# Kernel optimization log

Hardware: AMD Instinct MI355X
Metric: run time of the kernel (lower is better)

## Reference

```python
import jax, jax.numpy as jnp
import numpy as np


def setup_inputs() -> dict:
    key = jax.random.key(0)
    kq, kk, kv = jax.random.split(key, 3)
    B, L, H, E = 4, 2048, 16, 64
    return {
        "queries": jax.random.normal(kq, (B, L, H, E), dtype=jnp.float32),
        "keys": jax.random.normal(kk, (B, L, H, E), dtype=jnp.float32),
        "values": jax.random.normal(kv, (B, L, H, E), dtype=jnp.float32),
    }


def reference(queries, keys, values):
    B, L, H, E = queries.shape
    S = keys.shape[1]
    scale = 1.0 / jnp.sqrt(jnp.asarray(E, queries.dtype))
    # scores: [B, H, L, S]
    scores = jnp.einsum("blhe,bshe->bhls", queries, keys)
    # causal mask: disallow s > l (upper triangle, diagonal=1)
    causal = jnp.triu(jnp.ones((L, S), dtype=bool), k=1)
    scores = jnp.where(causal[None, None], -jnp.inf, scores)
    A = jax.nn.softmax(scale * scores, axis=-1)
    V = jnp.einsum("bhls,bshd->blhd", A, values)
    return V
```

## Files before the change

kernel.cpp:

```cpp
#include <hip/hip_runtime.h>
#include <hip/hip_bf16.h>

typedef __attribute__((ext_vector_type(8))) short short8;
typedef __attribute__((ext_vector_type(4))) float f32x4;
typedef __attribute__((ext_vector_type(4))) float f4;
typedef __attribute__((ext_vector_type(2))) unsigned uint2v;

#define MFMA(a, b, c) __builtin_amdgcn_mfma_f32_16x16x32_bf16(a, b, c, 0, 0, 0)

constexpr int B_ = 4, L = 2048, H = 16, E = 64;
constexpr int QBLK = 128, KVBLK = 64, NW = 8;
constexpr int LDP = 72;
constexpr float LOG2E = 1.4426950408889634f;
constexpr float C2 = 14.426950408889634f;
constexpr size_t NELEM = (size_t)B_ * L * H * E;
constexpr size_t WS_NEEDED = NELEM * 2 * 3;
constexpr int TILE_SHORTS = KVBLK * E;

__device__ __forceinline__ unsigned short f2bf(float f) {
  union { float f; unsigned u; } x;
  x.f = f;
  unsigned r = x.u + 0x7fffu + ((x.u >> 16) & 1u);
  return (unsigned short)(r >> 16);
}

__device__ __forceinline__ float exp2_fast(float x) {
  float r;
  asm("v_exp_f32 %0, %1" : "=v"(r) : "v"(x));
  return r;
}
__device__ __forceinline__ unsigned cvt_pk_bf16(float lo, float hi) {
  unsigned r;
  asm("v_cvt_pk_bf16_f32 %0, %1, %2" : "=v"(r) : "v"(lo), "v"(hi));
  return r;
}

__device__ __forceinline__ void gload_lds16(const void* g, void* l) {
  __builtin_amdgcn_global_load_lds(
      (const __attribute__((address_space(1))) unsigned*)g,
      (__attribute__((address_space(3))) unsigned*)l, 16, 0, 0);
}

__device__ __forceinline__ void stage_tile8(const unsigned short* gtile,
                                            unsigned short* ltile,
                                            int wid, int lane) {
  const unsigned qb = (unsigned)wid * 1024u + (unsigned)lane * 16u;
  const unsigned qs = qb ^ (((qb >> 7) & 7u) << 4);
  gload_lds16((const char*)gtile + qs, (char*)ltile + qb);
}

__device__ __forceinline__ short8 lds_frag(const unsigned short* ltile, int row, int slot) {
  const unsigned byte = (unsigned)row * 128u +
                        ((((unsigned)slot) ^ ((unsigned)row & 7u)) << 4);
  return *(const short8*)((const char*)ltile + byte);
}

__device__ __forceinline__ void barrier_raw() {
  __builtin_amdgcn_sched_barrier(0);
  __builtin_amdgcn_s_barrier();
  __builtin_amdgcn_sched_barrier(0);
}

__global__ __launch_bounds__(256)
void convert_qk(const float* __restrict__ Q, const float* __restrict__ K,
                unsigned short* __restrict__ Qb, unsigned short* __restrict__ Kb) {
  const bool isq = (blockIdx.y == 0);
  const float* in = isq ? Q : K;
  unsigned short* out = isq ? Qb : Kb;
  const float scale = isq ? (0.125f * LOG2E) : 1.0f;
  const size_t t = (size_t)blockIdx.x * 256 + threadIdx.x;
  const size_t row = t >> 3;
  const int e0 = ((int)t & 7) * 8;
  const int h = (int)(row % H);
  const size_t bl = row / H;
  const int l = (int)(bl % L);
  const int b = (int)(bl / L);
  f4 a = *(const f4*)(in + t * 8);
  f4 c = *(const f4*)(in + t * 8 + 4);
  short8 o;
  o[0] = (short)f2bf(a[0] * scale); o[1] = (short)f2bf(a[1] * scale);
  o[2] = (short)f2bf(a[2] * scale); o[3] = (short)f2bf(a[3] * scale);
  o[4] = (short)f2bf(c[0] * scale); o[5] = (short)f2bf(c[1] * scale);
  o[6] = (short)f2bf(c[2] * scale); o[7] = (short)f2bf(c[3] * scale);
  *(short8*)(out + (((size_t)b * H + h) * L + l) * E + e0) = o;
}

__global__ __launch_bounds__(256)
void transpose_v(const float* __restrict__ V, unsigned short* __restrict__ Vt) {
  const int blk = blockIdx.x;
  const int st = blk % (L / KVBLK);
  const int bh = blk / (L / KVBLK);
  const int h = bh % H, b = bh / H;
  __shared__ unsigned short Ts[E][KVBLK + 8];
  const int tid = threadIdx.x;
  const int r = tid >> 3, e0 = (tid & 7) * 8;
  const float* vp = V + (((size_t)b * L + st * KVBLK) * H + h) * E;
#pragma unroll
  for (int rr = 0; rr < 2; ++rr) {
    const int row = rr * 32 + r;
    f4 a = *(const f4*)(vp + (size_t)row * (H * E) + e0);
    f4 c = *(const f4*)(vp + (size_t)row * (H * E) + e0 + 4);
#pragma unroll
    for (int j = 0; j < 4; ++j) Ts[e0 + j][row] = f2bf(a[j]);
#pragma unroll
    for (int j = 0; j < 4; ++j) Ts[e0 + 4 + j][row] = f2bf(c[j]);
  }
  __syncthreads();
  const int e = tid >> 2, k0 = (tid & 3) * 16;
  unsigned short* op = Vt + ((size_t)bh * (L / KVBLK) + st) * (E * KVBLK) + e * KVBLK + k0;
  *(short8*)op = *(const short8*)&Ts[e][k0];
  *(short8*)(op + 8) = *(const short8*)&Ts[e][k0 + 8];
}

__global__ __launch_bounds__(512, 6)
void fattn3(const unsigned short* __restrict__ Qb, const unsigned short* __restrict__ Kb,
            const unsigned short* __restrict__ Vt, float* __restrict__ O) {
  const int bh = blockIdx.x;
  const int qtile = (int)(gridDim.y - 1) - blockIdx.y;
  const int b = bh >> 4, h = bh & 15;
  const int tid = threadIdx.x;
  const int wid = tid >> 6;
  const int lane = tid & 63;
  const int lg = lane >> 4, lm = lane & 15;
  const int qrow0 = qtile * QBLK + wid * 16;

  __shared__ __align__(16) unsigned short Ks[2][TILE_SHORTS];
  __shared__ __align__(16) unsigned short Vs[2][TILE_SHORTS];
  __shared__ __align__(16) unsigned short Pt[NW][16 * LDP];

  const unsigned short* qbase = Qb + ((size_t)bh * L + qrow0 + lm) * E + lg * 8;
  short8 qf0 = *(const short8*)qbase;
  short8 qf1 = *(const short8*)(qbase + 32);

  f32x4 o[4];
#pragma unroll
  for (int et = 0; et < 4; ++et) o[et] = (f32x4){0.f, 0.f, 0.f, 0.f};
  float lsum = 0.f;

  const unsigned short* kbase = Kb + (size_t)bh * L * E;
  const unsigned short* vbase = Vt + (size_t)bh * L * E;

  const int nkv = 2 * qtile + 2;
  const f32x4 cinit = (f32x4){-C2, -C2, -C2, -C2};

  stage_tile8(kbase, Ks[0], wid, lane);
  stage_tile8(vbase, Vs[0], wid, lane);

  for (int kt = 0; kt < nkv; ++kt) {
    const int cur = kt & 1, nxt = cur ^ 1;

    asm volatile("s_waitcnt lgkmcnt(0)" ::: "memory");
    barrier_raw();

    if (kt + 1 < nkv) {
      stage_tile8(kbase + (size_t)(kt + 1) * TILE_SHORTS, Ks[nxt], wid, lane);
      stage_tile8(vbase + (size_t)(kt + 1) * TILE_SHORTS, Vs[nxt], wid, lane);
      asm volatile("s_waitcnt vmcnt(2)" ::: "memory");
    } else {
      asm volatile("s_waitcnt vmcnt(0)" ::: "memory");
    }
    barrier_raw();

    const bool dead = (kt * KVBLK) > (qrow0 + 15);
    if (dead) continue;

    f32x4 stl[4];
#pragma unroll
    for (int ct = 0; ct < 4; ++ct) {
      short8 k0 = lds_frag(Ks[cur], ct * 16 + lm, lg);
      short8 k1 = lds_frag(Ks[cur], ct * 16 + lm, 4 + lg);
      f32x4 acc = cinit;
      acc = MFMA(k0, qf0, acc);
      acc = MFMA(k1, qf1, acc);
      stl[ct] = acc;
    }

    if (kt * KVBLK + KVBLK - 1 > qrow0) {
#pragma unroll
      for (int ct = 0; ct < 4; ++ct)
#pragma unroll
        for (int r = 0; r < 4; ++r) {
          const int key = kt * KVBLK + ct * 16 + lg * 4 + r;
          if (key > qrow0 + lm) stl[ct][r] = -1e30f;
        }
    }

#pragma unroll
    for (int ct = 0; ct < 4; ++ct)
#pragma unroll
      for (int r = 0; r < 4; ++r) {
        const float p = exp2_fast(stl[ct][r]);
        stl[ct][r] = p;
        lsum += p;
      }

#pragma unroll
    for (int ct = 0; ct < 4; ++ct) {
      uint2v w;
      w[0] = cvt_pk_bf16(stl[ct][0], stl[ct][1]);
      w[1] = cvt_pk_bf16(stl[ct][2], stl[ct][3]);
      *(uint2v*)&Pt[wid][lm * LDP + ct * 16 + lg * 4] = w;
    }
    short8 pf0 = *(const short8*)&Pt[wid][lm * LDP + 0 * 32 + lg * 8];
    short8 pf1 = *(const short8*)&Pt[wid][lm * LDP + 1 * 32 + lg * 8];

#pragma unroll
    for (int et = 0; et < 4; ++et) {
      short8 v0 = lds_frag(Vs[cur], et * 16 + lm, lg);
      short8 v1 = lds_frag(Vs[cur], et * 16 + lm, 4 + lg);
      o[et] = MFMA(pf0, v0, o[et]);
      o[et] = MFMA(pf1, v1, o[et]);
    }
  }

  lsum += __shfl_xor(lsum, 16);
  lsum += __shfl_xor(lsum, 32);
  float linv[4];
#pragma unroll
  for (int r = 0; r < 4; ++r) linv[r] = 1.f / __shfl(lsum, lg * 20 + r);
  float* op = O + (((size_t)b * L + qrow0 + lg * 4) * H + h) * E;
#pragma unroll
  for (int r = 0; r < 4; ++r)
#pragma unroll
    for (int et = 0; et < 4; ++et)
      op[(size_t)r * (H * E) + et * 16 + lm] = o[et][r] * linv[r];
}

constexpr int LDV_F = 72, LDP_F = 72;
__global__ __launch_bounds__(256, 2)
void fattn_v1(const float* __restrict__ Q, const float* __restrict__ K,
              const float* __restrict__ V, float* __restrict__ O) {
  const int qtile = blockIdx.x;
  const int bh = blockIdx.y;
  const int b = bh / H, h = bh % H;
  const int tid = threadIdx.x;
  const int wid = tid >> 6;
  const int lane = tid & 63;
  const int lg = lane >> 4, lm = lane & 15;
  __shared__ __align__(16) short Vs[E * LDV_F];
  __shared__ __align__(16) short Ps[4][16 * LDP_F];
  const int qrow0 = qtile * 64 + wid * 16;
  short8 qf[2];
  {
    const float* qp = Q + (((size_t)b * L + (qrow0 + lm)) * H + h) * E + lg * 8;
#pragma unroll
    for (int kc = 0; kc < 2; ++kc) {
      f4 a = *(const f4*)(qp + kc * 32);
      f4 c = *(const f4*)(qp + kc * 32 + 4);
      short8 r;
      r[0] = (short)f2bf(a[0] * 0.125f); r[1] = (short)f2bf(a[1] * 0.125f);
      r[2] = (short)f2bf(a[2] * 0.125f); r[3] = (short)f2bf(a[3] * 0.125f);
      r[4] = (short)f2bf(c[0] * 0.125f); r[5] = (short)f2bf(c[1] * 0.125f);
      r[6] = (short)f2bf(c[2] * 0.125f); r[7] = (short)f2bf(c[3] * 0.125f);
      qf[kc] = r;
    }
  }
  f32x4 o[4];
#pragma unroll
  for (int et = 0; et < 4; ++et) o[et] = (f32x4){0.f, 0.f, 0.f, 0.f};
  float mrow[4], lrow[4];
#pragma unroll
  for (int r = 0; r < 4; ++r) { mrow[r] = -1e30f; lrow[r] = 0.f; }
  const float* kbase = K + (((size_t)b * L) * H + h) * E;
  const float* vbase = V + (((size_t)b * L) * H + h) * E;
  const int nkv = qtile + 1;
  for (int kt = 0; kt < nkv; ++kt) {
    __syncthreads();
    {
      const int key = tid >> 2;
      const int eb = (tid & 3) * 16;
      const float* vp = vbase + (size_t)(kt * 64 + key) * (H * E) + eb;
#pragma unroll
      for (int i = 0; i < 4; ++i) {
        f4 v = *(const f4*)(vp + i * 4);
        Vs[(eb + i * 4 + 0) * LDV_F + key] = (short)f2bf(v[0]);
        Vs[(eb + i * 4 + 1) * LDV_F + key] = (short)f2bf(v[1]);
        Vs[(eb + i * 4 + 2) * LDV_F + key] = (short)f2bf(v[2]);
        Vs[(eb + i * 4 + 3) * LDV_F + key] = (short)f2bf(v[3]);
      }
    }
    f32x4 s[4];
#pragma unroll
    for (int ct = 0; ct < 4; ++ct) {
      f32x4 acc = (f32x4){0.f, 0.f, 0.f, 0.f};
      const float* kp = kbase + (size_t)(kt * 64 + ct * 16 + lm) * (H * E) + lg * 8;
#pragma unroll
      for (int kc = 0; kc < 2; ++kc) {
        f4 a = *(const f4*)(kp + kc * 32);
        f4 c = *(const f4*)(kp + kc * 32 + 4);
        short8 kf;
        kf[0] = (short)f2bf(a[0]); kf[1] = (short)f2bf(a[1]);
        kf[2] = (short)f2bf(a[2]); kf[3] = (short)f2bf(a[3]);
        kf[4] = (short)f2bf(c[0]); kf[5] = (short)f2bf(c[1]);
        kf[6] = (short)f2bf(c[2]); kf[7] = (short)f2bf(c[3]);
        acc = MFMA(qf[kc], kf, acc);
      }
      s[ct] = acc;
    }
    if (kt == nkv - 1) {
#pragma unroll
      for (int ct = 0; ct < 4; ++ct) {
        const int sg = kt * 64 + ct * 16 + lm;
#pragma unroll
        for (int r = 0; r < 4; ++r)
          if (sg > qrow0 + lg * 4 + r) s[ct][r] = -1e30f;
      }
    }
#pragma unroll
    for (int r = 0; r < 4; ++r) {
      float tm = fmaxf(fmaxf(s[0][r], s[1][r]), fmaxf(s[2][r], s[3][r]));
      tm = fmaxf(tm, __shfl_xor(tm, 1));
      tm = fmaxf(tm, __shfl_xor(tm, 2));
      tm = fmaxf(tm, __shfl_xor(tm, 4));
      tm = fmaxf(tm, __shfl_xor(tm, 8));
      const float mnew = fmaxf(mrow[r], tm);
      const float sc = __expf(mrow[r] - mnew);
      mrow[r] = mnew;
      float rs = 0.f;
#pragma unroll
      for (int ct = 0; ct < 4; ++ct) {
        const float p = __expf(s[ct][r] - mnew);
        s[ct][r] = p;
        rs += p;
      }
      rs += __shfl_xor(rs, 1);
      rs += __shfl_xor(rs, 2);
      rs += __shfl_xor(rs, 4);
      rs += __shfl_xor(rs, 8);
      lrow[r] = lrow[r] * sc + rs;
#pragma unroll
      for (int et = 0; et < 4; ++et) o[et][r] *= sc;
    }
#pragma unroll
    for (int ct = 0; ct < 4; ++ct)
#pragma unroll
      for (int r = 0; r < 4; ++r)
        Ps[wid][(lg * 4 + r) * LDP_F + ct * 16 + lm] = (short)f2bf(s[ct][r]);
    __syncthreads();
    short8 pf[2];
    pf[0] = *(const short8*)&Ps[wid][lm * LDP_F + 0 * 32 + lg * 8];
    pf[1] = *(const short8*)&Ps[wid][lm * LDP_F + 1 * 32 + lg * 8];
#pragma unroll
    for (int et = 0; et < 4; ++et)
#pragma unroll
      for (int kc = 0; kc < 2; ++kc) {
        short8 vf = *(const short8*)&Vs[(et * 16 + lm) * LDV_F + kc * 32 + lg * 8];
        o[et] = MFMA(pf[kc], vf, o[et]);
      }
  }
  float* op = O + (((size_t)b * L + qrow0) * H + h) * E;
#pragma unroll
  for (int r = 0; r < 4; ++r) {
    const float inv = 1.f / lrow[r];
#pragma unroll
    for (int et = 0; et < 4; ++et)
      op[(size_t)(lg * 4 + r) * (H * E) + et * 16 + lm] = o[et][r] * inv;
  }
}

extern "C" void kernel_launch(void* const* d_in, const int* in_sizes, int n_in,
                              void* d_out, int out_size, void* d_ws, size_t ws_size,
                              hipStream_t stream) {
  const float* Q = (const float*)d_in[0];
  const float* K = (const float*)d_in[1];
  const float* V = (const float*)d_in[2];
  float* Out = (float*)d_out;
  if (ws_size >= WS_NEEDED) {
    unsigned short* Qb = (unsigned short*)d_ws;
    unsigned short* Kb = Qb + NELEM;
    unsigned short* Vt = Kb + NELEM;
    dim3 gc((unsigned)(NELEM / (256 * 8)), 2);
    convert_qk<<<gc, 256, 0, stream>>>(Q, K, Qb, Kb);
    transpose_v<<<B_ * H * (L / KVBLK), 256, 0, stream>>>(V, Vt);
    dim3 grid(B_ * H, L / QBLK);
    fattn3<<<grid, 512, 0, stream>>>(Qb, Kb, Vt, Out);
  } else {
    dim3 grid(L / 64, B_ * H);
    fattn_v1<<<grid, 256, 0, stream>>>(Q, K, V, Out);
  }
}
```

Baseline: 76.52 us.

## Redistribute P fragments via lane shuffles instead of LDS round-trip

Replaces the per-wave LDS write/read that reshapes the softmax probability tile into MFMA A-operand layout with register-level packing and two rounds of cross-lane shuffles. This drops the Pt shared buffer, which lowers LDS footprint, and raises the occupancy hint in launch bounds from 6 to 8. The q-tile ordering across blockIdx.y is also permuted to interleave heavy and light causal tiles. The shuffles add ALU and DPP/permute work and more selects, and the higher occupancy hint may constrain registers.

Result: slower. 84.89 us (+10.9%).

```diff
diff --git a/kernel.cpp b/kernel.cpp
--- a/kernel.cpp
+++ b/kernel.cpp
@@ -4,13 +4,12 @@
 typedef __attribute__((ext_vector_type(8))) short short8;
 typedef __attribute__((ext_vector_type(4))) float f32x4;
 typedef __attribute__((ext_vector_type(4))) float f4;
-typedef __attribute__((ext_vector_type(2))) unsigned uint2v;
+typedef __attribute__((ext_vector_type(4))) unsigned uint4v;
 
 #define MFMA(a, b, c) __builtin_amdgcn_mfma_f32_16x16x32_bf16(a, b, c, 0, 0, 0)
 
 constexpr int B_ = 4, L = 2048, H = 16, E = 64;
-constexpr int QBLK = 128, KVBLK = 64, NW = 8;
-constexpr int LDP = 72;
+constexpr int QBLK = 128, KVBLK = 64;
 constexpr float LOG2E = 1.4426950408889634f;
 constexpr float C2 = 14.426950408889634f;
 constexpr size_t NELEM = (size_t)B_ * L * H * E;
@@ -112,11 +111,13 @@
   *(short8*)(op + 8) = *(const short8*)&Ts[e][k0 + 8];
 }
 
-__global__ __launch_bounds__(512, 6)
-void fattn3(const unsigned short* __restrict__ Qb, const unsigned short* __restrict__ Kb,
+__global__ __launch_bounds__(512, 8)
+void fattn4(const unsigned short* __restrict__ Qb, const unsigned short* __restrict__ Kb,
             const unsigned short* __restrict__ Vt, float* __restrict__ O) {
   const int bh = blockIdx.x;
-  const int qtile = (int)(gridDim.y - 1) - blockIdx.y;
+  const int y = blockIdx.y;
+  const int jr = 3 - (y >> 2);
+  const int qtile = 4 * ((jr + (y & 3)) & 3) + jr;
   const int b = bh >> 4, h = bh & 15;
   const int tid = threadIdx.x;
   const int wid = tid >> 6;
@@ -126,7 +127,6 @@
 
   __shared__ __align__(16) unsigned short Ks[2][TILE_SHORTS];
   __shared__ __align__(16) unsigned short Vs[2][TILE_SHORTS];
-  __shared__ __align__(16) unsigned short Pt[NW][16 * LDP];
 
   const unsigned short* qbase = Qb + ((size_t)bh * L + qrow0 + lm) * E + lg * 8;
   short8 qf0 = *(const short8*)qbase;
@@ -142,6 +142,9 @@
 
   const int nkv = 2 * qtile + 2;
   const f32x4 cinit = (f32x4){-C2, -C2, -C2, -C2};
+  const bool bg1 = (lg & 2) != 0;
+  const bool bg0 = (lg & 1) != 0;
+  const bool tt = (bg1 == bg0);
 
   stage_tile8(kbase, Ks[0], wid, lane);
   stage_tile8(vbase, Vs[0], wid, lane);
@@ -167,11 +170,11 @@
     f32x4 stl[4];
 #pragma unroll
     for (int ct = 0; ct < 4; ++ct) {
-      short8 k0 = lds_frag(Ks[cur], ct * 16 + lm, lg);
-      short8 k1 = lds_frag(Ks[cur], ct * 16 + lm, 4 + lg);
+      short8 k0f = lds_frag(Ks[cur], ct * 16 + lm, lg);
+      short8 k1f = lds_frag(Ks[cur], ct * 16 + lm, 4 + lg);
       f32x4 acc = cinit;
-      acc = MFMA(k0, qf0, acc);
-      acc = MFMA(k1, qf1, acc);
+      acc = MFMA(k0f, qf0, acc);
+      acc = MFMA(k1f, qf1, acc);
       stl[ct] = acc;
     }
 
@@ -194,15 +197,32 @@
         lsum += p;
       }
 
-#pragma unroll
-    for (int ct = 0; ct < 4; ++ct) {
-      uint2v w;
-      w[0] = cvt_pk_bf16(stl[ct][0], stl[ct][1]);
-      w[1] = cvt_pk_bf16(stl[ct][2], stl[ct][3]);
-      *(uint2v*)&Pt[wid][lm * LDP + ct * 16 + lg * 4] = w;
-    }
-    short8 pf0 = *(const short8*)&Pt[wid][lm * LDP + 0 * 32 + lg * 8];
-    short8 pf1 = *(const short8*)&Pt[wid][lm * LDP + 1 * 32 + lg * 8];
+    unsigned pkw0[4], pkw1[4];
+#pragma unroll
+    for (int c = 0; c < 4; ++c) {
+      pkw0[c] = cvt_pk_bf16(stl[c][0], stl[c][1]);
+      pkw1[c] = cvt_pk_bf16(stl[c][2], stl[c][3]);
+    }
+    unsigned o0 = bg1 ? pkw0[1] : pkw0[0];
+    unsigned o1 = bg1 ? pkw1[1] : pkw1[0];
+    unsigned o2 = bg1 ? pkw0[3] : pkw0[2];
+    unsigned o3 = bg1 ? pkw1[3] : pkw1[2];
+    unsigned rA0 = __shfl_xor(bg1 ? pkw0[0] : pkw0[1], 32);
+    unsigned rA1 = __shfl_xor(bg1 ? pkw1[0] : pkw1[1], 32);
+    unsigned rA2 = __shfl_xor(bg1 ? pkw0[2] : pkw0[3], 32);
+    unsigned rA3 = __shfl_xor(bg1 ? pkw1[2] : pkw1[3], 32);
+    unsigned kk0 = tt ? o0 : rA0;
+    unsigned kk1 = tt ? o1 : rA1;
+    unsigned kk2 = tt ? o2 : rA2;
+    unsigned kk3 = tt ? o3 : rA3;
+    unsigned rB0 = __shfl_xor(tt ? rA0 : o0, 16);
+    unsigned rB1 = __shfl_xor(tt ? rA1 : o1, 16);
+    unsigned rB2 = __shfl_xor(tt ? rA2 : o2, 16);
+    unsigned rB3 = __shfl_xor(tt ? rA3 : o3, 16);
+    uint4v u0 = { bg0 ? rB0 : kk0, bg0 ? rB1 : kk1, bg0 ? kk0 : rB0, bg0 ? kk1 : rB1 };
+    uint4v u1 = { bg0 ? rB2 : kk2, bg0 ? rB3 : kk3, bg0 ? kk2 : rB2, bg0 ? kk3 : rB3 };
+    short8 pf0 = __builtin_bit_cast(short8, u0);
+    short8 pf1 = __builtin_bit_cast(short8, u1);
 
 #pragma unroll
     for (int et = 0; et < 4; ++et) {
@@ -373,7 +393,7 @@
     convert_qk<<<gc, 256, 0, stream>>>(Q, K, Qb, Kb);
     transpose_v<<<B_ * H * (L / KVBLK), 256, 0, stream>>>(V, Vt);
     dim3 grid(B_ * H, L / QBLK);
-    fattn3<<<grid, 512, 0, stream>>>(Qb, Kb, Vt, Out);
+    fattn4<<<grid, 512, 0, stream>>>(Qb, Kb, Vt, Out);
   } else {
     dim3 grid(L / 64, B_ * H);
     fattn_v1<<<grid, 256, 0, stream>>>(Q, K, V, Out);
```

## Fuse Q/K convert and V transpose into one prep kernel; rebalance q-tile order

Applied to the files above, without the earlier changes.

Merges the Q/K bf16 conversion and V transpose kernels into a single launch with a 3-row grid, removing one kernel launch and its inter-kernel gap. The attention kernel remaps blockIdx.y to q-tiles with an interleaved order so heavy and light causal tiles are mixed across the dispatch, rather than strictly heaviest first. It also precomputes swizzled LDS fragment offsets outside the loop and unrolls the KV loop by 2 to cut address arithmetic. The fused prep launches many idle blocks in the V row, and the unroll may raise register pressure.

New measurement: 86.82 us. 13.5% more time.

```diff
diff --git a/kernel.cpp b/kernel.cpp
--- a/kernel.cpp
+++ b/kernel.cpp
@@ -43,16 +43,8 @@
 
 __device__ __forceinline__ void stage_tile8(const unsigned short* gtile,
                                             unsigned short* ltile,
-                                            int wid, int lane) {
-  const unsigned qb = (unsigned)wid * 1024u + (unsigned)lane * 16u;
-  const unsigned qs = qb ^ (((qb >> 7) & 7u) << 4);
+                                            unsigned qb, unsigned qs) {
   gload_lds16((const char*)gtile + qs, (char*)ltile + qb);
-}
-
-__device__ __forceinline__ short8 lds_frag(const unsigned short* ltile, int row, int slot) {
-  const unsigned byte = (unsigned)row * 128u +
-                        ((((unsigned)slot) ^ ((unsigned)row & 7u)) << 4);
-  return *(const short8*)((const char*)ltile + byte);
 }
 
 __device__ __forceinline__ void barrier_raw() {
@@ -62,37 +54,39 @@
 }
 
 __global__ __launch_bounds__(256)
-void convert_qk(const float* __restrict__ Q, const float* __restrict__ K,
-                unsigned short* __restrict__ Qb, unsigned short* __restrict__ Kb) {
-  const bool isq = (blockIdx.y == 0);
-  const float* in = isq ? Q : K;
-  unsigned short* out = isq ? Qb : Kb;
-  const float scale = isq ? (0.125f * LOG2E) : 1.0f;
-  const size_t t = (size_t)blockIdx.x * 256 + threadIdx.x;
-  const size_t row = t >> 3;
-  const int e0 = ((int)t & 7) * 8;
-  const int h = (int)(row % H);
-  const size_t bl = row / H;
-  const int l = (int)(bl % L);
-  const int b = (int)(bl / L);
-  f4 a = *(const f4*)(in + t * 8);
-  f4 c = *(const f4*)(in + t * 8 + 4);
-  short8 o;
-  o[0] = (short)f2bf(a[0] * scale); o[1] = (short)f2bf(a[1] * scale);
-  o[2] = (short)f2bf(a[2] * scale); o[3] = (short)f2bf(a[3] * scale);
-  o[4] = (short)f2bf(c[0] * scale); o[5] = (short)f2bf(c[1] * scale);
-  o[6] = (short)f2bf(c[2] * scale); o[7] = (short)f2bf(c[3] * scale);
-  *(short8*)(out + (((size_t)b * H + h) * L + l) * E + e0) = o;
-}
-
-__global__ __launch_bounds__(256)
-void transpose_v(const float* __restrict__ V, unsigned short* __restrict__ Vt) {
+void prep_all(const float* __restrict__ Q, const float* __restrict__ K,
+              const float* __restrict__ V,
+              unsigned short* __restrict__ Qb, unsigned short* __restrict__ Kb,
+              unsigned short* __restrict__ Vt) {
+  __shared__ unsigned short Ts[E][KVBLK + 8];
+  const int tid = threadIdx.x;
+  if (blockIdx.y < 2) {
+    const bool isq = (blockIdx.y == 0);
+    const float* in = isq ? Q : K;
+    unsigned short* out = isq ? Qb : Kb;
+    const float scale = isq ? (0.125f * LOG2E) : 1.0f;
+    const size_t t = (size_t)blockIdx.x * 256 + tid;
+    const size_t row = t >> 3;
+    const int e0 = ((int)t & 7) * 8;
+    const int h = (int)(row % H);
+    const size_t bl = row / H;
+    const int l = (int)(bl % L);
+    const int b = (int)(bl / L);
+    f4 a = *(const f4*)(in + t * 8);
+    f4 c = *(const f4*)(in + t * 8 + 4);
+    short8 o;
+    o[0] = (short)f2bf(a[0] * scale); o[1] = (short)f2bf(a[1] * scale);
+    o[2] = (short)f2bf(a[2] * scale); o[3] = (short)f2bf(a[3] * scale);
+    o[4] = (short)f2bf(c[0] * scale); o[5] = (short)f2bf(c[1] * scale);
+    o[6] = (short)f2bf(c[2] * scale); o[7] = (short)f2bf(c[3] * scale);
+    *(short8*)(out + (((size_t)b * H + h) * L + l) * E + e0) = o;
+    return;
+  }
   const int blk = blockIdx.x;
+  if (blk >= B_ * H * (L / KVBLK)) return;
   const int st = blk % (L / KVBLK);
   const int bh = blk / (L / KVBLK);
   const int h = bh % H, b = bh / H;
-  __shared__ unsigned short Ts[E][KVBLK + 8];
-  const int tid = threadIdx.x;
   const int r = tid >> 3, e0 = (tid & 7) * 8;
   const float* vp = V + (((size_t)b * L + st * KVBLK) * H + h) * E;
 #pragma unroll
@@ -116,7 +110,9 @@
 void fattn3(const unsigned short* __restrict__ Qb, const unsigned short* __restrict__ Kb,
             const unsigned short* __restrict__ Vt, float* __restrict__ O) {
   const int bh = blockIdx.x;
-  const int qtile = (int)(gridDim.y - 1) - blockIdx.y;
+  const int y = blockIdx.y;
+  const int jr = 3 - (y >> 2);
+  const int qtile = 4 * ((jr + (y & 3)) & 3) + jr;
   const int b = bh >> 4, h = bh & 15;
   const int tid = threadIdx.x;
   const int wid = tid >> 6;
@@ -128,6 +124,22 @@
   __shared__ __align__(16) unsigned short Vs[2][TILE_SHORTS];
   __shared__ __align__(16) unsigned short Pt[NW][16 * LDP];
 
+  int offA[4], offB[4];
+#pragma unroll
+  for (int ct = 0; ct < 4; ++ct) {
+    const int row = ct * 16 + lm;
+    offA[ct] = row * 128 + ((lg ^ (row & 7)) << 4);
+    offB[ct] = row * 128 + (((4 + lg) ^ (row & 7)) << 4);
+  }
+  int wrOff[4];
+#pragma unroll
+  for (int ct = 0; ct < 4; ++ct) wrOff[ct] = (lm * LDP + ct * 16 + lg * 4) * 2;
+  const int rdOff0 = (lm * LDP + lg * 8) * 2;
+  const int rdOff1 = (lm * LDP + 32 + lg * 8) * 2;
+  char* const ptw = (char*)Pt[wid];
+  const unsigned sqb = (unsigned)wid * 1024u + (unsigned)lane * 16u;
+  const unsigned sqs = sqb ^ (((sqb >> 7) & 7u) << 4);
+
   const unsigned short* qbase = Qb + ((size_t)bh * L + qrow0 + lm) * E + lg * 8;
   short8 qf0 = *(const short8*)qbase;
   short8 qf1 = *(const short8*)(qbase + 32);
@@ -143,9 +155,10 @@
   const int nkv = 2 * qtile + 2;
   const f32x4 cinit = (f32x4){-C2, -C2, -C2, -C2};
 
-  stage_tile8(kbase, Ks[0], wid, lane);
-  stage_tile8(vbase, Vs[0], wid, lane);
-
+  stage_tile8(kbase, Ks[0], sqb, sqs);
+  stage_tile8(vbase, Vs[0], sqb, sqs);
+
+#pragma unroll 2
   for (int kt = 0; kt < nkv; ++kt) {
     const int cur = kt & 1, nxt = cur ^ 1;
 
@@ -153,8 +166,8 @@
     barrier_raw();
 
     if (kt + 1 < nkv) {
-      stage_tile8(kbase + (size_t)(kt + 1) * TILE_SHORTS, Ks[nxt], wid, lane);
-      stage_tile8(vbase + (size_t)(kt + 1) * TILE_SHORTS, Vs[nxt], wid, lane);
+      stage_tile8(kbase + (size_t)(kt + 1) * TILE_SHORTS, Ks[nxt], sqb, sqs);
+      stage_tile8(vbase + (size_t)(kt + 1) * TILE_SHORTS, Vs[nxt], sqb, sqs);
       asm volatile("s_waitcnt vmcnt(2)" ::: "memory");
     } else {
       asm volatile("s_waitcnt vmcnt(0)" ::: "memory");
@@ -164,14 +177,17 @@
     const bool dead = (kt * KVBLK) > (qrow0 + 15);
     if (dead) continue;
 
+    const char* kl = (const char*)Ks[cur];
+    const char* vl = (const char*)Vs[cur];
+
     f32x4 stl[4];
 #pragma unroll
     for (int ct = 0; ct < 4; ++ct) {
-      short8 k0 = lds_frag(Ks[cur], ct * 16 + lm, lg);
-      short8 k1 = lds_frag(Ks[cur], ct * 16 + lm, 4 + lg);
+      short8 k0f = *(const short8*)(kl + offA[ct]);
+      short8 k1f = *(const short8*)(kl + offB[ct]);
       f32x4 acc = cinit;
-      acc = MFMA(k0, qf0, acc);
-      acc = MFMA(k1, qf1, acc);
+      acc = MFMA(k0f, qf0, acc);
+      acc = MFMA(k1f, qf1, acc);
       stl[ct] = acc;
     }
 
@@ -199,15 +215,15 @@
       uint2v w;
       w[0] = cvt_pk_bf16(stl[ct][0], stl[ct][1]);
       w[1] = cvt_pk_bf16(stl[ct][2], stl[ct][3]);
-      *(uint2v*)&Pt[wid][lm * LDP + ct * 16 + lg * 4] = w;
-    }
-    short8 pf0 = *(const short8*)&Pt[wid][lm * LDP + 0 * 32 + lg * 8];
-    short8 pf1 = *(const short8*)&Pt[wid][lm * LDP + 1 * 32 + lg * 8];
+      *(uint2v*)(ptw + wrOff[ct]) = w;
+    }
+    short8 pf0 = *(const short8*)(ptw + rdOff0);
+    short8 pf1 = *(const short8*)(ptw + rdOff1);
 
 #pragma unroll
     for (int et = 0; et < 4; ++et) {
-      short8 v0 = lds_frag(Vs[cur], et * 16 + lm, lg);
-      short8 v1 = lds_frag(Vs[cur], et * 16 + lm, 4 + lg);
+      short8 v0 = *(const short8*)(vl + offA[et]);
+      short8 v1 = *(const short8*)(vl + offB[et]);
       o[et] = MFMA(pf0, v0, o[et]);
       o[et] = MFMA(pf1, v1, o[et]);
     }
@@ -369,9 +385,8 @@
     unsigned short* Qb = (unsigned short*)d_ws;
     unsigned short* Kb = Qb + NELEM;
     unsigned short* Vt = Kb + NELEM;
-    dim3 gc((unsigned)(NELEM / (256 * 8)), 2);
-    convert_qk<<<gc, 256, 0, stream>>>(Q, K, Qb, Kb);
-    transpose_v<<<B_ * H * (L / KVBLK), 256, 0, stream>>>(V, Vt);
+    dim3 gp((unsigned)(NELEM / (256 * 8)), 3);
+    prep_all<<<gp, 256, 0, stream>>>(Q, K, V, Qb, Kb, Vt);
     dim3 grid(B_ * H, L / QBLK);
     fattn3<<<grid, 512, 0, stream>>>(Qb, Kb, Vt, Out);
   } else {
```
